# Performance work log

Hardware: AMD Instinct MI355X
Metric: run time of the kernel (lower is better)

The kernel has to match this reference:

```python
import jax, jax.numpy as jnp
import numpy as np
from math import sqrt

B, S, E, H = 2, 2048, 1024, 16

def setup_inputs() -> dict:
    key = jax.random.key(0)
    k1, k2, k3, k4, k5 = jax.random.split(key, 5)
    bound_in = 1.0 / sqrt(E)
    return {
        "inputs": jax.random.normal(k1, (B, S, E), dtype=jnp.float32),
        "W_in": jax.random.uniform(k2, (3 * E, E), dtype=jnp.float32, minval=-bound_in, maxval=bound_in),
        "b_in": jax.random.uniform(k3, (3 * E,), dtype=jnp.float32, minval=-bound_in, maxval=bound_in),
        "W_out": jax.random.uniform(k4, (E, E), dtype=jnp.float32, minval=-bound_in, maxval=bound_in),
        "b_out": jax.random.uniform(k5, (E,), dtype=jnp.float32, minval=-bound_in, maxval=bound_in),
    }

def reference(inputs, W_in, b_in, W_out, b_out):
    # Eval-mode forward (dropout is identity when not training).
    b, s, e = inputs.shape
    hd = e // H
    qkv = jnp.einsum('bse,fe->bsf', inputs, W_in) + b_in  # [B,S,3E]
    q, k, v = jnp.split(qkv, 3, axis=-1)
    # [B,S,E] -> [B,H,S,hd]
    to_heads = lambda t: t.reshape(b, s, H, hd).transpose(0, 2, 1, 3)
    q, k, v = to_heads(q), to_heads(k), to_heads(v)
    scores = jnp.einsum('bhqd,bhkd->bhqk', q, k) / jnp.sqrt(jnp.float32(hd))
    causal = jnp.tril(jnp.ones((s, s), dtype=bool))
    scores = jnp.where(causal, scores, -jnp.inf)
    attn = jax.nn.softmax(scores, axis=-1)  # stable max-subtract softmax, same math
    out = jnp.einsum('bhqk,bhkd->bhqd', attn, v)  # [B,H,S,hd]
    out = out.transpose(0, 2, 1, 3).reshape(b, s, e)
    return jnp.einsum('bse,fe->bsf', out, W_out) + b_out
```

## Files before the change

kernel.cpp:

```cpp
#include <hip/hip_runtime.h>
#include <hip/hip_bf16.h>
#include <stdint.h>

#define SS 2048
#define EE 1024
#define HH 16
#define HD 64

#define QSCALE 0.1803368801111137f

typedef __attribute__((ext_vector_type(8))) short short8;
typedef __attribute__((ext_vector_type(4))) float f32x4;

__device__ __forceinline__ short f2bf(float f) {
  union { float f; uint32_t u; } x; x.f = f;
  uint32_t r = x.u + 0x7fffu + ((x.u >> 16) & 1u);
  return (short)(r >> 16);
}

__device__ __forceinline__ uint32_t pk_bf16(float a, float b) {
#if __has_builtin(__builtin_amdgcn_cvt_pk_bf16_f32)
  typedef __attribute__((ext_vector_type(2))) __bf16 bf16x2_t;
  union { bf16x2_t v; uint32_t u; } x;
  x.v = __builtin_amdgcn_cvt_pk_bf16_f32(a, b);
  return x.u;
#else
  return (uint32_t)(uint16_t)f2bf(a) | ((uint32_t)(uint16_t)f2bf(b) << 16);
#endif
}

#if __has_builtin(__builtin_amdgcn_exp2f)
#define EXP2F __builtin_amdgcn_exp2f
#else
#define EXP2F exp2f
#endif

__device__ __forceinline__ void async_cp16(const void* g, void* l) {
  __builtin_amdgcn_global_load_lds((const __attribute__((address_space(1))) void*)g,
                                   (__attribute__((address_space(3))) void*)l, 16, 0, 0);
}

#define N4_X  1048576
#define N4_W1 786432
#define N4_W2 262144
__global__ __launch_bounds__(256) void cvt_all(
    const float* __restrict__ x, const float* __restrict__ w1,
    const float* __restrict__ w2,
    short* __restrict__ xb, short* __restrict__ w1b, short* __restrict__ w2b)
{
  int i = blockIdx.x * 256 + threadIdx.x;
  const float* src; short* dst; int off;
  if (i < N4_X)            { src = x;  dst = xb;  off = i; }
  else if (i < N4_X+N4_W1) { src = w1; dst = w1b; off = i - N4_X; }
  else                     { src = w2; dst = w2b; off = i - N4_X - N4_W1; }
  float4 v = *(const float4*)&src[(size_t)off * 4];
  uint2 pk;
  pk.x = pk_bf16(v.x, v.y);
  pk.y = pk_bf16(v.z, v.w);
  *(uint2*)&dst[(size_t)off * 4] = pk;
}

__global__ __launch_bounds__(256) void gemm_qkv(
    const short* __restrict__ A, const short* __restrict__ Bw,
    const float* __restrict__ bias,
    short* __restrict__ qw, short* __restrict__ kw, short* __restrict__ vw,
    int M, int N, int K)
{
  __shared__ short smem[17408];
  const int tid = threadIdx.x;
  const int lane = tid & 63;
  const int wv = tid >> 6;
  const int wm = (wv >> 1) * 64;
  const int wn = (wv & 1) * 64;
  const int t = lane >> 4;
  const int lr = lane & 15;
  const int bm = blockIdx.y * 128;
  const int bn = blockIdx.x * 128;

  f32x4 acc[4][4];
  #pragma unroll
  for (int i = 0; i < 4; ++i)
    #pragma unroll
    for (int j = 0; j < 4; ++j) acc[i][j] = (f32x4){0.f, 0.f, 0.f, 0.f};

  auto stage = [&](int buf, int k0) {
    short* sA = smem + buf * 8192;
    short* sB = smem + buf * 8192 + 4096;
    #pragma unroll
    for (int it = 0; it < 2; ++it) {
      int c = it * 256 + wv * 64 + lane;
      int row = c >> 2;
      int ch = (c & 3) * 8;
      async_cp16(&A[(size_t)(bm + row) * K + k0 + ch],
                 (char*)sA + (size_t)(it * 256 + wv * 64) * 16);
      async_cp16(&Bw[(size_t)(bn + row) * K + k0 + ch],
                 (char*)sB + (size_t)(it * 256 + wv * 64) * 16);
    }
  };

  const int nk = K >> 5;
  stage(0, 0);
  __syncthreads();

  for (int k = 0; k < nk; ++k) {
    if (k + 1 < nk) stage((k + 1) & 1, (k + 1) << 5);
    const short* cA = smem + (k & 1) * 8192;
    const short* cB = smem + (k & 1) * 8192 + 4096;
    short8 af[4], bfr[4];
    #pragma unroll
    for (int i = 0; i < 4; ++i) af[i] = *(const short8*)&cA[(wm + i*16 + lr)*32 + t*8];
    #pragma unroll
    for (int j = 0; j < 4; ++j) bfr[j] = *(const short8*)&cB[(wn + j*16 + lr)*32 + t*8];
    #pragma unroll
    for (int i = 0; i < 4; ++i)
      #pragma unroll
      for (int j = 0; j < 4; ++j)
        acc[i][j] = __builtin_amdgcn_mfma_f32_16x16x32_bf16(af[i], bfr[j], acc[i][j], 0, 0, 0);
    __syncthreads();
  }

  short* vx = smem;
  const bool isV = (bn >= 2048);
  const bool isQ = (bn < 1024);
  int b_ = bm >> 11;
  int s0 = bm & 2047;
  if (isV) {
    #pragma unroll
    for (int i = 0; i < 4; ++i) {
      int row0 = wm + i*16 + t*4;
      #pragma unroll
      for (int j = 0; j < 4; ++j) {
        int cl = wn + j*16 + lr;
        float bv = bias[bn + cl];
        #pragma unroll
        for (int r = 0; r < 4; ++r)
          vx[cl*136 + row0 + r] = f2bf(acc[i][j][r] + bv);
      }
    }
    __syncthreads();
    int h0 = (bn - 2048) >> 6;
    #pragma unroll
    for (int it = 0; it < 8; ++it) {
      int cc = it * 256 + tid;
      int cl = cc >> 4;
      int ck = cc & 15;
      int h = h0 + (cl >> 6);
      int d = cl & 63;
      int f = ck >> 2, tt = ck & 3;
      const short* src = &vx[cl*136 + 32*f + 4*tt];
      uint2 lo = *(const uint2*)src;
      uint2 hi = *(const uint2*)(src + 16);
      uint4 val; val.x = lo.x; val.y = lo.y; val.z = hi.x; val.w = hi.y;
      *(uint4*)&vw[((size_t)(b_*HH + h)*HD + d)*SS + s0 + ck*8] = val;
    }
  } else {
    #pragma unroll
    for (int i = 0; i < 4; ++i) {
      int row0 = wm + i*16 + t*4;
      #pragma unroll
      for (int j = 0; j < 4; ++j) {
        int cl = wn + j*16 + lr;
        float bv = bias[bn + cl];
        #pragma unroll
        for (int r = 0; r < 4; ++r) {
          float v = acc[i][j][r] + bv;
          if (isQ) v *= QSCALE;
          vx[(row0 + r)*136 + cl] = f2bf(v);
        }
      }
    }
    __syncthreads();
    short* dst = isQ ? qw : kw;
    int h0 = (bn & 1023) >> 6;
    #pragma unroll
    for (int it = 0; it < 8; ++it) {
      int cc = it * 256 + tid;
      int row = cc >> 4;
      int ck = cc & 15;
      int h = h0 + (ck >> 3);
      int d0 = (ck & 7) * 8;
      *(uint4*)&dst[((size_t)(b_*HH + h)*SS + s0 + row)*HD + d0] =
          *(const uint4*)&vx[row*136 + ck*8];
    }
  }
}

__global__ __launch_bounds__(256) void gemm_out(
    const short* __restrict__ A, const short* __restrict__ Bw,
    const float* __restrict__ bias,
    float* __restrict__ C,
    int M, int N, int K)
{
  __shared__ short smem[12288];
  const int tid = threadIdx.x;
  const int lane = tid & 63;
  const int wv = tid >> 6;
  const int wm = (wv >> 1) * 32;
  const int wn = (wv & 1) * 64;
  const int t = lane >> 4;
  const int lr = lane & 15;
  const int bm = blockIdx.y * 64;
  const int bn = blockIdx.x * 128;

  f32x4 acc[2][4];
  #pragma unroll
  for (int i = 0; i < 2; ++i)
    #pragma unroll
    for (int j = 0; j < 4; ++j) acc[i][j] = (f32x4){0.f, 0.f, 0.f, 0.f};

  auto stage = [&](int buf, int k0) {
    short* sA = smem + buf * 6144;
    short* sB = smem + buf * 6144 + 2048;
    {
      int c = wv * 64 + lane;
      int row = c >> 2;
      int ch = (c & 3) * 8;
      async_cp16(&A[(size_t)(bm + row) * K + k0 + ch],
                 (char*)sA + (size_t)(wv * 64) * 16);
    }
    #pragma unroll
    for (int it = 0; it < 2; ++it) {
      int c = it * 256 + wv * 64 + lane;
      int row = c >> 2;
      int ch = (c & 3) * 8;
      async_cp16(&Bw[(size_t)(bn + row) * K + k0 + ch],
                 (char*)sB + (size_t)(it * 256 + wv * 64) * 16);
    }
  };

  const int nk = K >> 5;
  stage(0, 0);
  __syncthreads();

  for (int k = 0; k < nk; ++k) {
    if (k + 1 < nk) stage((k + 1) & 1, (k + 1) << 5);
    const short* cA = smem + (k & 1) * 6144;
    const short* cB = smem + (k & 1) * 6144 + 2048;
    short8 af[2], bfr[4];
    #pragma unroll
    for (int i = 0; i < 2; ++i) af[i] = *(const short8*)&cA[(wm + i*16 + lr)*32 + t*8];
    #pragma unroll
    for (int j = 0; j < 4; ++j) bfr[j] = *(const short8*)&cB[(wn + j*16 + lr)*32 + t*8];
    #pragma unroll
    for (int i = 0; i < 2; ++i)
      #pragma unroll
      for (int j = 0; j < 4; ++j)
        acc[i][j] = __builtin_amdgcn_mfma_f32_16x16x32_bf16(af[i], bfr[j], acc[i][j], 0, 0, 0);
    __syncthreads();
  }

  #pragma unroll
  for (int i = 0; i < 2; ++i) {
    int row0 = bm + wm + i*16 + t*4;
    #pragma unroll
    for (int j = 0; j < 4; ++j) {
      int col = bn + wn + j*16 + lr;
      float bv = bias[col];
      #pragma unroll
      for (int r = 0; r < 4; ++r)
        C[(size_t)(row0 + r) * N + col] = acc[i][j][r] + bv;
    }
  }
}

template<int MODE, typename TA>
__global__ __launch_bounds__(256) void gemm_bt(
    const TA* __restrict__ A, const float* __restrict__ Bw,
    const float* __restrict__ bias,
    float* __restrict__ C,
    short* __restrict__ qw, short* __restrict__ kw, short* __restrict__ vw,
    int M, int N, int K)
{
  __shared__ short sA[128*32];
  __shared__ short sB[128*32];
  const int tid = threadIdx.x;
  const int lane = tid & 63;
  const int wv = tid >> 6;
  const int wm = (wv >> 1) * 64;
  const int wn = (wv & 1) * 64;
  const int t = lane >> 4;
  const int lr = lane & 15;
  const int bm = blockIdx.y * 128;
  const int bn = blockIdx.x * 128;

  f32x4 acc[4][4];
  #pragma unroll
  for (int i = 0; i < 4; ++i)
    #pragma unroll
    for (int j = 0; j < 4; ++j) acc[i][j] = (f32x4){0.f, 0.f, 0.f, 0.f};

  for (int k0 = 0; k0 < K; k0 += 32) {
    __syncthreads();
    if constexpr (sizeof(TA) == 4) {
      #pragma unroll
      for (int it = 0; it < 4; ++it) {
        int c = it * 256 + tid;
        int row = c >> 3, ch = (c & 7) * 4;
        float4 va = *(const float4*)&A[(size_t)(bm + row)*K + k0 + ch];
        uint2 pk; pk.x = pk_bf16(va.x, va.y); pk.y = pk_bf16(va.z, va.w);
        *(uint2*)&sA[row*32 + ch] = pk;
      }
    } else {
      #pragma unroll
      for (int it = 0; it < 2; ++it) {
        int c = it * 256 + tid;
        int row = c >> 2, ch = (c & 3) * 8;
        *(uint4*)&sA[row*32 + ch] = *(const uint4*)&A[(size_t)(bm + row)*K + k0 + ch];
      }
    }
    #pragma unroll
    for (int it = 0; it < 4; ++it) {
      int c = it * 256 + tid;
      int row = c >> 3, ch = (c & 7) * 4;
      float4 vb = *(const float4*)&Bw[(size_t)(bn + row)*K + k0 + ch];
      uint2 pk; pk.x = pk_bf16(vb.x, vb.y); pk.y = pk_bf16(vb.z, vb.w);
      *(uint2*)&sB[row*32 + ch] = pk;
    }
    __syncthreads();
    short8 af[4], bfr[4];
    #pragma unroll
    for (int i = 0; i < 4; ++i) af[i] = *(const short8*)&sA[(wm + i*16 + lr)*32 + t*8];
    #pragma unroll
    for (int j = 0; j < 4; ++j) bfr[j] = *(const short8*)&sB[(wn + j*16 + lr)*32 + t*8];
    #pragma unroll
    for (int i = 0; i < 4; ++i)
      #pragma unroll
      for (int j = 0; j < 4; ++j)
        acc[i][j] = __builtin_amdgcn_mfma_f32_16x16x32_bf16(af[i], bfr[j], acc[i][j], 0, 0, 0);
  }

  #pragma unroll
  for (int i = 0; i < 4; ++i) {
    int row0 = bm + wm + i*16 + t*4;
    #pragma unroll
    for (int j = 0; j < 4; ++j) {
      int col = bn + wn + j*16 + lr;
      float bv = bias[col];
      #pragma unroll
      for (int r = 0; r < 4; ++r) {
        float v = acc[i][j][r] + bv;
        int rr = row0 + r;
        if (MODE == 0) {
          C[(size_t)rr * N + col] = v;
        } else {
          int which = col >> 10;
          int e = col & 1023;
          int h = e >> 6, d = e & 63;
          int b_ = rr >> 11, s = rr & 2047;
          if (which == 0)
            qw[((size_t)(b_*HH + h)*SS + s)*HD + d] = f2bf(v * QSCALE);
          else if (which == 1)
            kw[((size_t)(b_*HH + h)*SS + s)*HD + d] = f2bf(v);
          else {
            int k7 = s & 127;
            int sp = (k7 & 0x60) | ((k7 & 0x0C) << 1) | ((k7 & 0x10) >> 2) | (k7 & 3);
            vw[((size_t)(b_*HH + h)*HD + d)*SS + (s & ~127) + sp] = f2bf(v);
          }
        }
      }
    }
  }
}

__global__ __launch_bounds__(512) void attn_kernel(
    const short* __restrict__ Q, const short* __restrict__ K,
    const short* __restrict__ Vt, short* __restrict__ O)
{
  __shared__ short sK[2][128*64];
  __shared__ short sV[2][64*128];
  const int tid = threadIdx.x;
  const int lane = tid & 63;
  const int w = tid >> 6;
  const int t = lane >> 4;
  const int lr = lane & 15;
  const int blk = blockIdx.x;
  const int qt = (blk < 256) ? (blk >> 5) : (15 - ((blk - 256) >> 5));
  const int bh = blk & 31;
  const int b = bh >> 4, h = bh & 15;
  const short* Qb = Q  + (size_t)bh * SS * HD;
  const short* Kb = K  + (size_t)bh * SS * HD;
  const short* Vb = Vt + (size_t)bh * HD * SS;
  const int qrow0 = qt * 128 + w * 16;

  auto stage = [&](int buf, int kb) {
    #pragma unroll
    for (int it2 = 0; it2 < 2; ++it2) {
      int s = it2 * 512 + tid;
      int krow = s >> 3;
      int kcc = (s & 7) ^ (krow & 7);
      async_cp16(&Kb[(size_t)(kb + krow) * HD + kcc * 8],
                 (char*)sK[buf] + (size_t)(it2 * 512 + w * 64) * 16);
      int d = s >> 4;
      int vcc = (s & 15) ^ (d & 15);
      async_cp16(&Vb[(size_t)d * SS + kb + vcc * 8],
                 (char*)sV[buf] + (size_t)(it2 * 512 + w * 64) * 16);
    }
  };

  short8 qf[2];
  #pragma unroll
  for (int st = 0; st < 2; ++st)
    qf[st] = *(const short8*)&Qb[(size_t)(qrow0 + lr) * HD + st*32 + t*8];

  f32x4 o[4];
  #pragma unroll
  for (int jd = 0; jd < 4; ++jd) o[jd] = (f32x4){0.f, 0.f, 0.f, 0.f};
  float l = 0.f;

  const int niter = qt + 1;
  stage(0, 0);
  __syncthreads();
  int cur = 0;

  #pragma unroll 1
  for (int it = 0; it < niter; ++it) {
    const int kb = it * 128;
    if (it + 1 < niter) stage(cur ^ 1, kb + 128);
    const short* sKc = sK[cur];
    const short* sVc = sV[cur];

    f32x4 sc[8];
    #pragma unroll
    for (int c = 0; c < 8; ++c) sc[c] = (f32x4){0.f,0.f,0.f,0.f};
    __builtin_amdgcn_s_setprio(1);
    #pragma unroll
    for (int c = 0; c < 8; ++c) {
      int krow = c*16 + lr;
      #pragma unroll
      for (int st = 0; st < 2; ++st) {
        int slot = krow*8 + ((st*4 + t) ^ (lr & 7));
        short8 kf = *(const short8*)&sKc[slot*8];
        sc[c] = __builtin_amdgcn_mfma_f32_16x16x32_bf16(kf, qf[st], sc[c], 0, 0, 0);
      }
    }
    __builtin_amdgcn_s_setprio(0);

    if (it == niter - 1) {
      int qg = qrow0 + lr;
      #pragma unroll
      for (int c = 0; c < 8; ++c)
        #pragma unroll
        for (int r = 0; r < 4; ++r)
          if (kb + c*16 + t*4 + r > qg) sc[c][r] = -1e30f;
    }

    float rs = 0.f;
    #pragma unroll
    for (int c = 0; c < 8; ++c)
      #pragma unroll
      for (int r = 0; r < 4; ++r) {
        sc[c][r] = EXP2F(sc[c][r]);
        rs += sc[c][r];
      }
    rs += __shfl_xor(rs, 16);
    rs += __shfl_xor(rs, 32);
    l += rs;

    __builtin_amdgcn_s_setprio(1);
    #pragma unroll
    for (int f = 0; f < 4; ++f) {
      union { uint32_t u[4]; short8 s8; } up;
      up.u[0] = pk_bf16(sc[2*f  ][0], sc[2*f  ][1]);
      up.u[1] = pk_bf16(sc[2*f  ][2], sc[2*f  ][3]);
      up.u[2] = pk_bf16(sc[2*f+1][0], sc[2*f+1][1]);
      up.u[3] = pk_bf16(sc[2*f+1][2], sc[2*f+1][3]);
      short8 pf = up.s8;
      #pragma unroll
      for (int jd = 0; jd < 4; ++jd) {
        int d = jd*16 + lr;
        int vslot = d*16 + ((f*4 + t) ^ lr);
        short8 vf = *(const short8*)&sVc[vslot*8];
        o[jd] = __builtin_amdgcn_mfma_f32_16x16x32_bf16(vf, pf, o[jd], 0, 0, 0);
      }
    }
    __builtin_amdgcn_s_setprio(0);

    __syncthreads();
    cur ^= 1;
  }

  float linv = 1.0f / l;
  size_t rowoff = ((size_t)(b * SS + qrow0 + lr)) * EE + h * HD;
  #pragma unroll
  for (int jd = 0; jd < 4; ++jd) {
    uint2 pw;
    pw.x = pk_bf16(o[jd][0] * linv, o[jd][1] * linv);
    pw.y = pk_bf16(o[jd][2] * linv, o[jd][3] * linv);
    *(uint2*)&O[rowoff + jd*16 + t*4] = pw;
  }
}

extern "C" void kernel_launch(void* const* d_in, const int* in_sizes, int n_in,
                              void* d_out, int out_size, void* d_ws, size_t ws_size,
                              hipStream_t stream) {
  const float* X     = (const float*)d_in[0];
  const float* W_in  = (const float*)d_in[1];
  const float* b_in  = (const float*)d_in[2];
  const float* W_out = (const float*)d_in[3];
  const float* b_out = (const float*)d_in[4];
  float* out = (float*)d_out;

  char* ws = (char*)d_ws;
  const size_t MB = 1024 * 1024;
  const int M = 2 * SS;

  if (ws_size >= 48 * MB) {
    short* Xb   = (short*)(ws);
    short* Wb1  = (short*)(ws + 8  * MB);
    short* Wb2  = (short*)(ws + 14 * MB);
    short* q_ws = (short*)(ws + 16 * MB);
    short* k_ws = (short*)(ws + 24 * MB);
    short* v_ws = (short*)(ws + 32 * MB);
    short* attn = (short*)(ws + 40 * MB);

    cvt_all<<<8192, 256, 0, stream>>>(X, W_in, W_out, Xb, Wb1, Wb2);
    gemm_qkv<<<dim3(24, 32), 256, 0, stream>>>(
        Xb, Wb1, b_in, q_ws, k_ws, v_ws, M, 3 * EE, EE);
    attn_kernel<<<dim3(512), 512, 0, stream>>>(q_ws, k_ws, v_ws, attn);
    gemm_out<<<dim3(8, 64), 256, 0, stream>>>(
        attn, Wb2, b_out, out, M, EE, EE);
  } else {
    short* q_ws = (short*)(ws);
    short* k_ws = (short*)(ws + 8  * MB);
    short* v_ws = (short*)(ws + 16 * MB);
    short* attn = (short*)(ws + 24 * MB);

    gemm_bt<1, float><<<dim3(24, 32), 256, 0, stream>>>(
        X, W_in, b_in, nullptr, q_ws, k_ws, v_ws, M, 3 * EE, EE);
    attn_kernel<<<dim3(512), 512, 0, stream>>>(q_ws, k_ws, v_ws, attn);
    gemm_bt<0, short><<<dim3(8, 32), 256, 0, stream>>>(
        attn, W_out, b_out, out, nullptr, nullptr, nullptr, M, EE, EE);
  }
}
```

Baseline: 179.5 us.

## Swap MFMA operands for vectorized epilogue stores and swizzle GEMM block order

In the Q/K path of the QKV GEMM and in the output GEMM, the MFMA A/B operands are swapped so each lane holds four consecutive output columns. This lets the epilogue add bias with a float4 load and write packed bf16x4 or float4 values directly to global memory. The Q/K path no longer stages through shared memory and drops a barrier. Block indices are also remapped with a stride-8 swizzle so that blocks running at the same time share A/B tiles in cache. The cost is an extra branch around the MFMA loop, and the swizzle's benefit depends on how the hardware schedules blocks.

Result: slower. 190.1 us (+5.9%).

```diff
diff --git a/kernel.cpp b/kernel.cpp
--- a/kernel.cpp
+++ b/kernel.cpp
@@ -74,8 +74,10 @@
   const int wn = (wv & 1) * 64;
   const int t = lane >> 4;
   const int lr = lane & 15;
-  const int bm = blockIdx.y * 128;
-  const int bn = blockIdx.x * 128;
+  const int wgid = blockIdx.y * 24 + blockIdx.x;
+  const int sw = (wgid & 7) * 96 + (wgid >> 3);
+  const int bm = (sw / 24) * 128;
+  const int bn = (sw % 24) * 128;
 
   f32x4 acc[4][4];
   #pragma unroll
@@ -98,6 +100,8 @@
     }
   };
 
+  const bool isV = (bn >= 2048);
+  const bool isQ = (bn < 1024);
   const int nk = K >> 5;
   stage(0, 0);
   __syncthreads();
@@ -111,20 +115,26 @@
     for (int i = 0; i < 4; ++i) af[i] = *(const short8*)&cA[(wm + i*16 + lr)*32 + t*8];
     #pragma unroll
     for (int j = 0; j < 4; ++j) bfr[j] = *(const short8*)&cB[(wn + j*16 + lr)*32 + t*8];
-    #pragma unroll
-    for (int i = 0; i < 4; ++i)
-      #pragma unroll
-      for (int j = 0; j < 4; ++j)
-        acc[i][j] = __builtin_amdgcn_mfma_f32_16x16x32_bf16(af[i], bfr[j], acc[i][j], 0, 0, 0);
+    if (isV) {
+      #pragma unroll
+      for (int i = 0; i < 4; ++i)
+        #pragma unroll
+        for (int j = 0; j < 4; ++j)
+          acc[i][j] = __builtin_amdgcn_mfma_f32_16x16x32_bf16(af[i], bfr[j], acc[i][j], 0, 0, 0);
+    } else {
+      #pragma unroll
+      for (int i = 0; i < 4; ++i)
+        #pragma unroll
+        for (int j = 0; j < 4; ++j)
+          acc[i][j] = __builtin_amdgcn_mfma_f32_16x16x32_bf16(bfr[j], af[i], acc[i][j], 0, 0, 0);
+    }
     __syncthreads();
   }
 
-  short* vx = smem;
-  const bool isV = (bn >= 2048);
-  const bool isQ = (bn < 1024);
   int b_ = bm >> 11;
   int s0 = bm & 2047;
   if (isV) {
+    short* vx = smem;
     #pragma unroll
     for (int i = 0; i < 4; ++i) {
       int row0 = wm + i*16 + t*4;
@@ -154,33 +164,27 @@
       *(uint4*)&vw[((size_t)(b_*HH + h)*HD + d)*SS + s0 + ck*8] = val;
     }
   } else {
-    #pragma unroll
-    for (int i = 0; i < 4; ++i) {
-      int row0 = wm + i*16 + t*4;
-      #pragma unroll
-      for (int j = 0; j < 4; ++j) {
-        int cl = wn + j*16 + lr;
-        float bv = bias[bn + cl];
-        #pragma unroll
-        for (int r = 0; r < 4; ++r) {
-          float v = acc[i][j][r] + bv;
-          if (isQ) v *= QSCALE;
-          vx[(row0 + r)*136 + cl] = f2bf(v);
-        }
-      }
-    }
-    __syncthreads();
     short* dst = isQ ? qw : kw;
-    int h0 = (bn & 1023) >> 6;
-    #pragma unroll
-    for (int it = 0; it < 8; ++it) {
-      int cc = it * 256 + tid;
-      int row = cc >> 4;
-      int ck = cc & 15;
-      int h = h0 + (ck >> 3);
-      int d0 = (ck & 7) * 8;
-      *(uint4*)&dst[((size_t)(b_*HH + h)*SS + s0 + row)*HD + d0] =
-          *(const uint4*)&vx[row*136 + ck*8];
+    #pragma unroll
+    for (int j = 0; j < 4; ++j) {
+      int ncol = bn + wn + j*16 + t*4;
+      float4 bv4 = *(const float4*)&bias[ncol];
+      int h = (ncol & 1023) >> 6;
+      int d0 = ncol & 63;
+      size_t base = ((size_t)(b_*HH + h) * SS) * HD + d0;
+      #pragma unroll
+      for (int i = 0; i < 4; ++i) {
+        int s = s0 + wm + i*16 + lr;
+        float v0 = acc[i][j][0] + bv4.x;
+        float v1 = acc[i][j][1] + bv4.y;
+        float v2 = acc[i][j][2] + bv4.z;
+        float v3 = acc[i][j][3] + bv4.w;
+        if (isQ) { v0 *= QSCALE; v1 *= QSCALE; v2 *= QSCALE; v3 *= QSCALE; }
+        uint2 pw;
+        pw.x = pk_bf16(v0, v1);
+        pw.y = pk_bf16(v2, v3);
+        *(uint2*)&dst[base + (size_t)s * HD] = pw;
+      }
     }
   }
 }
@@ -199,8 +203,10 @@
   const int wn = (wv & 1) * 64;
   const int t = lane >> 4;
   const int lr = lane & 15;
-  const int bm = blockIdx.y * 64;
-  const int bn = blockIdx.x * 128;
+  const int wgid = blockIdx.y * 8 + blockIdx.x;
+  const int sw = (wgid & 7) * 64 + (wgid >> 3);
+  const int bm = (sw >> 3) * 64;
+  const int bn = (sw & 7) * 128;
 
   f32x4 acc[2][4];
   #pragma unroll
@@ -245,20 +251,23 @@
     for (int i = 0; i < 2; ++i)
       #pragma unroll
       for (int j = 0; j < 4; ++j)
-        acc[i][j] = __builtin_amdgcn_mfma_f32_16x16x32_bf16(af[i], bfr[j], acc[i][j], 0, 0, 0);
+        acc[i][j] = __builtin_amdgcn_mfma_f32_16x16x32_bf16(bfr[j], af[i], acc[i][j], 0, 0, 0);
     __syncthreads();
   }
 
   #pragma unroll
-  for (int i = 0; i < 2; ++i) {
-    int row0 = bm + wm + i*16 + t*4;
-    #pragma unroll
-    for (int j = 0; j < 4; ++j) {
-      int col = bn + wn + j*16 + lr;
-      float bv = bias[col];
-      #pragma unroll
-      for (int r = 0; r < 4; ++r)
-        C[(size_t)(row0 + r) * N + col] = acc[i][j][r] + bv;
+  for (int j = 0; j < 4; ++j) {
+    int col = bn + wn + j*16 + t*4;
+    float4 bv4 = *(const float4*)&bias[col];
+    #pragma unroll
+    for (int i = 0; i < 2; ++i) {
+      int row = bm + wm + i*16 + lr;
+      float4 o4;
+      o4.x = acc[i][j][0] + bv4.x;
+      o4.y = acc[i][j][1] + bv4.y;
+      o4.z = acc[i][j][2] + bv4.z;
+      o4.w = acc[i][j][3] + bv4.w;
+      *(float4*)&C[(size_t)row * N + col] = o4;
     }
   }
 }
```
